# Kernel tuning notes

Measured on AMD Instinct MI355X. Metric: run time of the kernel, lower is better.

Reference implementation:

```python
import jax, jax.numpy as jnp
import numpy as np

N_S, N_G, E = 4000, 50000, 250000   # sample nodes, gene nodes, edges per relation
D, H, C1, C3 = 128, 4, 32, 64       # input dim, heads, layer-1 per-head dim, layer-3 per-head dim
NEG_SLOPE = 0.2


def gatv2(x_src, x_dst, src, dst, ea, Wl, bl, Wr, br, We, att, bias, n_dst, concat):
    """PyG GATv2Conv (add_self_loops=False, edge_dim=1, eval mode)."""
    Hh, C = att.shape
    xl = (x_src @ Wl + bl).reshape(-1, Hh, C)          # [N_src, H, C]
    xr = (x_dst @ Wr + br).reshape(-1, Hh, C)          # [N_dst, H, C]
    ee = (ea @ We).reshape(-1, Hh, C)                  # [E, H, C]
    m = jax.nn.leaky_relu(xl[src] + xr[dst] + ee, NEG_SLOPE)   # [E, H, C]
    logits = jnp.einsum('ehc,hc->eh', m, att)          # [E, H]
    # segment softmax over incoming edges of each destination node
    lmax = jax.ops.segment_max(logits, dst, num_segments=n_dst)[dst]
    ex = jnp.exp(logits - lmax)
    denom = jax.ops.segment_sum(ex, dst, num_segments=n_dst)[dst]
    alpha = ex / denom                                 # [E, H]
    out = jax.ops.segment_sum(xl[src] * alpha[:, :, None], dst, num_segments=n_dst)  # [N_dst, H, C]
    out = out.reshape(n_dst, Hh * C) if concat else out.mean(axis=1)
    return out + bias


def setup_inputs() -> dict:
    key = jax.random.key(0)
    ks = jax.random.split(key, 40)
    p = lambda i, shape: jax.random.normal(ks[i], shape, dtype=jnp.float32) * 0.05
    HC1, HC3 = H * C1, H * C3
    inp = {
        'x_mrna': p(0, (N_S, D)),
        'x_gene': p(1, (N_G, D)),
        'sg_src': jax.random.randint(ks[2], (E,), 0, N_S),
        'sg_dst': jax.random.randint(ks[3], (E,), 0, N_G),
        'gs_src': jax.random.randint(ks[4], (E,), 0, N_G),
        'gs_dst': jax.random.randint(ks[5], (E,), 0, N_S),
        'ea_sg': p(6, (E, 1)),
        'ea_gs': p(7, (E, 1)),
        # layer-1 GATv2 params, relation mrna->gene
        'Wl1_sg': p(8, (D, HC1)), 'bl1_sg': p(9, (HC1,)),
        'Wr1_sg': p(10, (D, HC1)), 'br1_sg': p(11, (HC1,)),
        'We1_sg': p(12, (1, HC1)), 'att1_sg': p(13, (H, C1)), 'bo1_sg': p(14, (HC1,)),
        # layer-1 GATv2 params, relation gene->mrna
        'Wl1_gs': p(15, (D, HC1)), 'bl1_gs': p(16, (HC1,)),
        'Wr1_gs': p(17, (D, HC1)), 'br1_gs': p(18, (HC1,)),
        'We1_gs': p(19, (1, HC1)), 'att1_gs': p(20, (H, C1)), 'bo1_gs': p(21, (HC1,)),
        # layer-3 GATv2 params, relation gene->mrna (concat=False)
        'Wl3_gs': p(22, (HC1, HC3)), 'bl3_gs': p(23, (HC3,)),
        'Wr3_gs': p(24, (HC1, HC3)), 'br3_gs': p(25, (HC3,)),
        'We3_gs': p(26, (1, HC3)), 'att3_gs': p(27, (H, C3)), 'bo3_gs': p(28, (C3,)),
        # self-loop linears for omic ('mrna') nodes
        'Wsl1': p(29, (D, C1)), 'bsl1': p(30, (C1,)),
        'Wsl3': p(31, (HC1, C3)), 'bsl3': p(32, (C3,)),
    }
    return inp


def reference(x_mrna, x_gene, sg_src, sg_dst, gs_src, gs_dst, ea_sg, ea_gs,
              Wl1_sg, bl1_sg, Wr1_sg, br1_sg, We1_sg, att1_sg, bo1_sg,
              Wl1_gs, bl1_gs, Wr1_gs, br1_gs, We1_gs, att1_gs, bo1_gs,
              Wl3_gs, bl3_gs, Wr3_gs, br3_gs, We3_gs, att3_gs, bo3_gs,
              Wsl1, bsl1, Wsl3, bsl3):
    # ---- layer 1 (HeteroConv over both relations) ----
    x1_gene = gatv2(x_mrna, x_gene, sg_src, sg_dst, ea_sg,
                    Wl1_sg, bl1_sg, Wr1_sg, br1_sg, We1_sg, att1_sg, bo1_sg, N_G, True)
    x1_mrna = gatv2(x_gene, x_mrna, gs_src, gs_dst, ea_gs,
                    Wl1_gs, bl1_gs, Wr1_gs, br1_gs, We1_gs, att1_gs, bo1_gs, N_S, True)
    # self-loop linear on omic nodes, repeated across heads (repeat(1, heads))
    x1_mrna = x1_mrna + jnp.tile(x_mrna @ Wsl1 + bsl1, (1, H))
    x1_mrna = jax.nn.relu(x1_mrna)
    x1_gene = jax.nn.relu(x1_gene)
    # ---- three_layers=False: x2 = x1; layer 3 (concat=False, head mean) ----
    x3_mrna = gatv2(x1_gene, x1_mrna, gs_src, gs_dst, ea_gs,
                    Wl3_gs, bl3_gs, Wr3_gs, br3_gs, We3_gs, att3_gs, bo3_gs, N_S, False)
    x3_mrna = x3_mrna + (x1_mrna @ Wsl3 + bsl3)
    x3_mrna = jax.nn.relu(x3_mrna)
    # integrator=None, single omic view -> squeeze to [N_S, C3]
    return x3_mrna
```

## Files before the change

### kernel.cpp

```cpp
#include <hip/hip_runtime.h>
#include <cstdint>
#include <cstddef>

#define NS 4000
#define NG 50000
#define NE 250000
#define DIM 128
#define NDST_TOT (NG + NS)

typedef __bf16 bf16_t;
typedef bf16_t bf16x8 __attribute__((ext_vector_type(8)));
typedef bf16_t bf16x4 __attribute__((ext_vector_type(4)));
typedef bf16_t bf16x2 __attribute__((ext_vector_type(2)));
typedef float floatx4 __attribute__((ext_vector_type(4)));

#define HIST_B 977
#define WT_TOT 143360
#define XM_W 64000
#define XG_W 800000
#define PREP_B 3935
struct HPArgs {
  const int* sgd; const int* gsd;
  int* cnt; unsigned short* rank_sg; unsigned short* rank_gs;
  const float* W[8]; bf16_t* Wt[8]; int N[8]; int e0[8];
  const float* xm; bf16_t* xbm;
  const float* xg; bf16_t* xbg;
};

__global__ __launch_bounds__(256) void histprep(HPArgs a) {
  if (blockIdx.x < HIST_B) {
    int e = blockIdx.x * 256 + threadIdx.x;
    if (e < NE) {
      a.rank_sg[e] = (unsigned short)atomicAdd(a.cnt + a.sgd[e], 1);
      a.rank_gs[e] = (unsigned short)atomicAdd(a.cnt + NG + a.gsd[e], 1);
    }
  } else {
    int u = (blockIdx.x - HIST_B) * 256 + threadIdx.x;
    if (u < WT_TOT) {
      int c = 0;
#pragma unroll
      for (int i = 1; i < 8; i++) if (u >= a.e0[i]) c = i;
      int idx = u - a.e0[c];
      int N = a.N[c];
      int k = idx / N, n = idx - k * N;
      a.Wt[c][n * 128 + k] = (bf16_t)a.W[c][idx];
    } else if (u < WT_TOT + XM_W) {
      int j = (u - WT_TOT) * 8;
      float4 v0 = *reinterpret_cast<const float4*>(a.xm + j);
      float4 v1 = *reinterpret_cast<const float4*>(a.xm + j + 4);
      bf16x8 b;
      b[0] = (bf16_t)v0.x; b[1] = (bf16_t)v0.y; b[2] = (bf16_t)v0.z; b[3] = (bf16_t)v0.w;
      b[4] = (bf16_t)v1.x; b[5] = (bf16_t)v1.y; b[6] = (bf16_t)v1.z; b[7] = (bf16_t)v1.w;
      *reinterpret_cast<bf16x8*>(a.xbm + j) = b;
    } else {
      int j = (u - WT_TOT - XM_W) * 8;
      float4 v0 = *reinterpret_cast<const float4*>(a.xg + j);
      float4 v1 = *reinterpret_cast<const float4*>(a.xg + j + 4);
      bf16x8 b;
      b[0] = (bf16_t)v0.x; b[1] = (bf16_t)v0.y; b[2] = (bf16_t)v0.z; b[3] = (bf16_t)v0.w;
      b[4] = (bf16_t)v1.x; b[5] = (bf16_t)v1.y; b[6] = (bf16_t)v1.z; b[7] = (bf16_t)v1.w;
      *reinterpret_cast<bf16x8*>(a.xbg + j) = b;
    }
  }
}

__global__ __launch_bounds__(1024) void scan1(const int* __restrict__ cnt,
                                              int* __restrict__ rp,
                                              int* __restrict__ csum, int n) {
  __shared__ int wsum[16];
  int i = blockIdx.x * 1024 + threadIdx.x;
  int lane = threadIdx.x & 63, w = threadIdx.x >> 6;
  int v = (i < n) ? cnt[i] : 0;
  int x = v;
#pragma unroll
  for (int off = 1; off < 64; off <<= 1) {
    int y = __shfl_up(x, off);
    if (lane >= off) x += y;
  }
  if (lane == 63) wsum[w] = x;
  __syncthreads();
  if (w == 0 && lane < 16) {
    int s = wsum[lane];
#pragma unroll
    for (int off = 1; off < 16; off <<= 1) {
      int y = __shfl_up(s, off);
      if (lane >= off) s += y;
    }
    wsum[lane] = s;
  }
  __syncthreads();
  int incl = x + (w ? wsum[w - 1] : 0);
  if (i < n) rp[i] = incl - v;
  if (threadIdx.x == 1023) csum[blockIdx.x] = incl;
}

__global__ __launch_bounds__(1024) void scan3(int* __restrict__ rp,
                                              const int* __restrict__ csum, int n) {
  __shared__ int pfx_s;
  if (threadIdx.x < 64) {
    int lane = threadIdx.x;
    int v = (lane < (int)blockIdx.x) ? csum[lane] : 0;
#pragma unroll
    for (int off = 32; off > 0; off >>= 1) v += __shfl_down(v, off);
    if (lane == 0) pfx_s = v;
  }
  __syncthreads();
  int i = blockIdx.x * 1024 + threadIdx.x;
  if (i < n) rp[i] += pfx_s;
  if (i == 0) rp[n] = 2 * NE;
}

#define SCAT_HALF 245
#define SCAT_B 490
struct SGArgs {
  const int* sgd; const int* gsd; const int* sgs; const int* gss;
  const float* easg; const float* eags;
  const int* rp; const unsigned short* rank_sg; const unsigned short* rank_gs;
  uint2* meta;
  const bf16_t* X[5];
  const bf16_t* Wt[5];
  const float* Bv[5];
  bf16_t* Y[5];
  int M[5];
  int Ncol[5];
  int blk0[5];
};

__global__ __launch_bounds__(256) void scatgemm(SGArgs a) {
  if (blockIdx.x < SCAT_B) {
    int rel = (int)blockIdx.x >= SCAT_HALF;
    int b = (int)blockIdx.x - (rel ? SCAT_HALF : 0);
    int t4 = (b * 256 + (int)threadIdx.x) * 4;
    if (t4 < NE) {
      const int* dp = rel ? a.gsd : a.sgd;
      const int* sp = rel ? a.gss : a.sgs;
      const float* ep = rel ? a.eags : a.easg;
      const unsigned short* rk = rel ? a.rank_gs : a.rank_sg;
      const int* rpb = a.rp + (rel ? NG : 0);
      int4 d4 = *reinterpret_cast<const int4*>(dp + t4);
      int4 s4 = *reinterpret_cast<const int4*>(sp + t4);
      float4 e4 = *reinterpret_cast<const float4*>(ep + t4);
      ushort4 r4 = *reinterpret_cast<const ushort4*>(rk + t4);
      int p0 = rpb[d4.x] + (int)r4.x;
      int p1 = rpb[d4.y] + (int)r4.y;
      int p2 = rpb[d4.z] + (int)r4.z;
      int p3 = rpb[d4.w] + (int)r4.w;
      uint2 v0, v1, v2, v3;
      v0.x = (unsigned)s4.x; v0.y = __float_as_uint(e4.x);
      v1.x = (unsigned)s4.y; v1.y = __float_as_uint(e4.y);
      v2.x = (unsigned)s4.z; v2.y = __float_as_uint(e4.z);
      v3.x = (unsigned)s4.w; v3.y = __float_as_uint(e4.w);
      a.meta[p0] = v0;
      a.meta[p1] = v1;
      a.meta[p2] = v2;
      a.meta[p3] = v3;
    }
    return;
  }
  int bid = blockIdx.x - SCAT_B;
  int c = 0;
#pragma unroll
  for (int i = 1; i < 5; i++) if (bid >= a.blk0[i]) c = i;
  const bf16_t* X = a.X[c];
  const bf16_t* Wt = a.Wt[c];
  const float* B = a.Bv[c];
  bf16_t* Y = a.Y[c];
  int M = a.M[c];
  int N = a.Ncol[c];

  int wv = threadIdx.x >> 6, lane = threadIdx.x & 63;
  int m16 = lane & 15, quad = lane >> 4;
  int row0 = (bid - a.blk0[c]) * 64 + wv * 16;
  int arow = row0 + m16;
  const bf16_t* xp = X + (size_t)arow * DIM + quad * 8;

  bf16x8 afrag[4];
#pragma unroll
  for (int kk = 0; kk < 4; kk++) {
    bf16x8 av = {};
    if (arow < M) av = *reinterpret_cast<const bf16x8*>(xp + kk * 32);
    afrag[kk] = av;
  }

  int ncols = N >> 4;
  for (int nt = 0; nt < ncols; nt++) {
    int col = nt * 16 + m16;
    const bf16_t* bptr = Wt + (size_t)col * DIM + quad * 8;
    floatx4 acc = {0.f, 0.f, 0.f, 0.f};
#pragma unroll
    for (int kk = 0; kk < 4; kk++) {
      bf16x8 b = *reinterpret_cast<const bf16x8*>(bptr + kk * 32);
      acc = __builtin_amdgcn_mfma_f32_16x16x32_bf16(afrag[kk], b, acc, 0, 0, 0);
    }
    float bias = B[col];
    int orow = row0 + quad * 4;
#pragma unroll
    for (int r = 0; r < 4; r++)
      if (orow + r < M) Y[(size_t)(orow + r) * N + col] = (bf16_t)(acc[r] + bias);
  }
}

template <int NCFG>
struct GArgs {
  const bf16_t* X[NCFG];
  const bf16_t* Wt[NCFG];
  const float* Bv[NCFG];
  bf16_t* Y[NCFG];
  int M[NCFG];
  int Ncol[NCFG];
  int blk0[NCFG];
};

template <int NCFG>
__global__ __launch_bounds__(256) void gemm_multi(GArgs<NCFG> a) {
  int c = 0;
#pragma unroll
  for (int i = 1; i < NCFG; i++) if ((int)blockIdx.x >= a.blk0[i]) c = i;
  const bf16_t* X = a.X[c];
  const bf16_t* Wt = a.Wt[c];
  const float* B = a.Bv[c];
  bf16_t* Y = a.Y[c];
  int M = a.M[c];
  int N = a.Ncol[c];

  int wv = threadIdx.x >> 6, lane = threadIdx.x & 63;
  int m16 = lane & 15, quad = lane >> 4;
  int row0 = (blockIdx.x - a.blk0[c]) * 64 + wv * 16;
  int arow = row0 + m16;
  const bf16_t* xp = X + (size_t)arow * DIM + quad * 8;

  bf16x8 afrag[4];
#pragma unroll
  for (int kk = 0; kk < 4; kk++) {
    bf16x8 av = {};
    if (arow < M) av = *reinterpret_cast<const bf16x8*>(xp + kk * 32);
    afrag[kk] = av;
  }

  int ncols = N >> 4;
  for (int nt = 0; nt < ncols; nt++) {
    int col = nt * 16 + m16;
    const bf16_t* bptr = Wt + (size_t)col * DIM + quad * 8;
    floatx4 acc = {0.f, 0.f, 0.f, 0.f};
#pragma unroll
    for (int kk = 0; kk < 4; kk++) {
      bf16x8 b = *reinterpret_cast<const bf16x8*>(bptr + kk * 32);
      acc = __builtin_amdgcn_mfma_f32_16x16x32_bf16(afrag[kk], b, acc, 0, 0, 0);
    }
    float bias = B[col];
    int orow = row0 + quad * 4;
#pragma unroll
    for (int r = 0; r < 4; r++)
      if (orow + r < M) Y[(size_t)(orow + r) * N + col] = (bf16_t)(acc[r] + bias);
  }
}

#define SGB 3125
__global__ __launch_bounds__(256) void gatC(
    const int* __restrict__ rp, const uint2* __restrict__ meta,
    const float* __restrict__ WeS, const float* __restrict__ attS,
    const float* __restrict__ boS,
    const bf16_t* __restrict__ xlS, const bf16_t* __restrict__ xrS,
    bf16_t* __restrict__ outS,
    const float* __restrict__ WeG, const float* __restrict__ attG,
    const float* __restrict__ boG,
    const bf16_t* __restrict__ xlG, const bf16_t* __restrict__ xrG,
    const bf16_t* __restrict__ slG, bf16_t* __restrict__ outG) {
  __shared__ uint2 smeta[256];
  __shared__ float lacc[16][128];
  __shared__ float lden[16][4];
  int lane = threadIdx.x & 63, wv = threadIdx.x >> 6;
  int gl = lane & 15, grp = lane >> 4;

  if (blockIdx.x < SGB) {
    int wid = blockIdx.x * 4 + wv;
    int d0 = wid * 4;
    int q = lane < 5 ? lane : 0;
    int rv = rp[d0 + q];
    int beg = __shfl(rv, grp), end = __shfl(rv, grp + 1);
    int dst = d0 + grp;

    float wev[8], atv[8], xrv[8], acc[8];
    *reinterpret_cast<float4*>(wev) = *reinterpret_cast<const float4*>(WeS + gl * 8);
    *reinterpret_cast<float4*>(wev + 4) = *reinterpret_cast<const float4*>(WeS + gl * 8 + 4);
    *reinterpret_cast<float4*>(atv) = *reinterpret_cast<const float4*>(attS + gl * 8);
    *reinterpret_cast<float4*>(atv + 4) = *reinterpret_cast<const float4*>(attS + gl * 8 + 4);
    bf16x8 xrb = *reinterpret_cast<const bf16x8*>(xrS + (size_t)dst * 128 + gl * 8);
#pragma unroll
    for (int v = 0; v < 8; v++) { xrv[v] = (float)xrb[v]; acc[v] = 0.f; }
    float den = 0.f;

    for (int i0 = beg; i0 < end; i0 += 16) {
      int cnt = min(16, end - i0);
      int s_l = 0; float ea_l = 0.f;
      if (gl < cnt) {
        uint2 mv = meta[i0 + gl];
        s_l = (int)mv.x; ea_l = __uint_as_float(mv.y);
      }
      int base = lane & 48;
      float ea = __shfl(ea_l, base);
      bf16x8 xlb = *reinterpret_cast<const bf16x8*>(
          xlS + (size_t)__shfl(s_l, base) * 128 + gl * 8);
      for (int k = 0; k < cnt; k++) {
        bf16x8 cur = xlb;
        float eac = ea;
        if (k + 1 < cnt) {
          ea = __shfl(ea_l, base + k + 1);
          xlb = *reinterpret_cast<const bf16x8*>(
              xlS + (size_t)__shfl(s_l, base + k + 1) * 128 + gl * 8);
        }
        float p = 0.f, xf[8];
#pragma unroll
        for (int v = 0; v < 8; v++) {
          xf[v] = (float)cur[v];
          float z = fmaf(eac, wev[v], xrv[v]) + xf[v];
          z = z > 0.f ? z : 0.2f * z;
          p = fmaf(z, atv[v], p);
        }
        p += __shfl_xor(p, 1);
        p += __shfl_xor(p, 2);
        float ex = __expf(p);
        den += ex;
#pragma unroll
        for (int v = 0; v < 8; v++) acc[v] = fmaf(ex, xf[v], acc[v]);
      }
    }
    float inv = den > 0.f ? 1.f / den : 0.f;
    bf16x8 o;
#pragma unroll
    for (int v = 0; v < 8; v++) {
      float val = acc[v] * inv + boS[gl * 8 + v];
      o[v] = (bf16_t)(val > 0.f ? val : 0.f);
    }
    *reinterpret_cast<bf16x8*>(outS + (size_t)dst * 128 + gl * 8) = o;
  } else {
    int d = (int)blockIdx.x - SGB;
    const int* rpg = rp + NG;
    int G = wv * 4 + grp;
    int tid = threadIdx.x;

    float wev[8], atv[8], xrv[8], acc[8];
    *reinterpret_cast<float4*>(wev) = *reinterpret_cast<const float4*>(WeG + gl * 8);
    *reinterpret_cast<float4*>(wev + 4) = *reinterpret_cast<const float4*>(WeG + gl * 8 + 4);
    *reinterpret_cast<float4*>(atv) = *reinterpret_cast<const float4*>(attG + gl * 8);
    *reinterpret_cast<float4*>(atv + 4) = *reinterpret_cast<const float4*>(attG + gl * 8 + 4);
    bf16x8 xrb = *reinterpret_cast<const bf16x8*>(xrG + (size_t)d * 128 + gl * 8);
#pragma unroll
    for (int v = 0; v < 8; v++) { xrv[v] = (float)xrb[v]; acc[v] = 0.f; }
    float den = 0.f;

    int beg = rpg[d], end = rpg[d + 1];
    for (int base = beg; base < end; base += 256) {
      int cntb = min(256, end - base);
      __syncthreads();
      if (tid < cntb) smeta[tid] = meta[base + tid];
      __syncthreads();
      int e = G;
      uint2 mv; bf16x8 xlb;
      if (e < cntb) {
        mv = smeta[e];
        xlb = *reinterpret_cast<const bf16x8*>(xlG + (size_t)mv.x * 128 + gl * 8);
      }
      while (e < cntb) {
        bf16x8 cur = xlb;
        float eac = __uint_as_float(mv.y);
        int en = e + 16;
        if (en < cntb) {
          mv = smeta[en];
          xlb = *reinterpret_cast<const bf16x8*>(xlG + (size_t)mv.x * 128 + gl * 8);
        }
        float p = 0.f, xf[8];
#pragma unroll
        for (int v = 0; v < 8; v++) {
          xf[v] = (float)cur[v];
          float z = fmaf(eac, wev[v], xrv[v]) + xf[v];
          z = z > 0.f ? z : 0.2f * z;
          p = fmaf(z, atv[v], p);
        }
        p += __shfl_xor(p, 1);
        p += __shfl_xor(p, 2);
        float ex = __expf(p);
        den += ex;
#pragma unroll
        for (int v = 0; v < 8; v++) acc[v] = fmaf(ex, xf[v], acc[v]);
        e = en;
      }
    }
#pragma unroll
    for (int v = 0; v < 8; v++) lacc[G][gl * 8 + v] = acc[v];
    if ((gl & 3) == 0) lden[G][gl >> 2] = den;
    __syncthreads();
    if (wv != 0) return;
    int ch = lane * 2;
    int h = lane >> 4;
    float a0 = 0.f, a1 = 0.f, dh = 0.f;
#pragma unroll
    for (int g2 = 0; g2 < 16; g2++) {
      a0 += lacc[g2][ch];
      a1 += lacc[g2][ch + 1];
      dh += lden[g2][h];
    }
    float inv = dh > 0.f ? 1.f / dh : 0.f;
    float v0 = a0 * inv + boG[ch] + (float)slG[(size_t)d * 32 + (ch & 31)];
    float v1 = a1 * inv + boG[ch + 1] + (float)slG[(size_t)d * 32 + ((ch + 1) & 31)];
    bf16x2 o;
    o[0] = (bf16_t)(v0 > 0.f ? v0 : 0.f);
    o[1] = (bf16_t)(v1 > 0.f ? v1 : 0.f);
    *reinterpret_cast<bf16x2*>(outG + (size_t)d * 128 + ch) = o;
  }
}

__global__ __launch_bounds__(256) void gatE(
    const int* __restrict__ rp, const uint2* __restrict__ meta,
    const float* __restrict__ We, const float* __restrict__ att,
    const bf16_t* __restrict__ xl, const bf16_t* __restrict__ xr,
    const float* __restrict__ bo, const bf16_t* __restrict__ sl,
    float* __restrict__ out) {
  __shared__ uint2 smeta[256];
  __shared__ float lacc[16][256];
  __shared__ float lden[16][4];
  int lane = threadIdx.x & 63, wv = threadIdx.x >> 6;
  int gl = lane & 15, grp = lane >> 4;
  int G = wv * 4 + grp;
  int tid = threadIdx.x;
  int d = blockIdx.x;

  float wev[16], atv[16], xrv[16], acc[16];
#pragma unroll
  for (int b = 0; b < 4; b++) {
    *reinterpret_cast<float4*>(wev + b * 4) =
        *reinterpret_cast<const float4*>(We + gl * 16 + b * 4);
    *reinterpret_cast<float4*>(atv + b * 4) =
        *reinterpret_cast<const float4*>(att + gl * 16 + b * 4);
  }
  {
    bf16x8 r0 = *reinterpret_cast<const bf16x8*>(xr + (size_t)d * 256 + gl * 16);
    bf16x8 r1 = *reinterpret_cast<const bf16x8*>(xr + (size_t)d * 256 + gl * 16 + 8);
#pragma unroll
    for (int v = 0; v < 8; v++) { xrv[v] = (float)r0[v]; xrv[v + 8] = (float)r1[v]; }
  }
#pragma unroll
  for (int v = 0; v < 16; v++) acc[v] = 0.f;
  float den = 0.f;

  int beg = rp[d], end = rp[d + 1];
  for (int base = beg; base < end; base += 256) {
    int cntb = min(256, end - base);
    __syncthreads();
    if (tid < cntb) smeta[tid] = meta[base + tid];
    __syncthreads();
    int e = G;
    uint2 mv; bf16x8 x0, x1;
    if (e < cntb) {
      mv = smeta[e];
      x0 = *reinterpret_cast<const bf16x8*>(xl + (size_t)mv.x * 256 + gl * 16);
      x1 = *reinterpret_cast<const bf16x8*>(xl + (size_t)mv.x * 256 + gl * 16 + 8);
    }
    while (e < cntb) {
      bf16x8 c0 = x0, c1 = x1;
      float eac = __uint_as_float(mv.y);
      int en = e + 16;
      if (en < cntb) {
        mv = smeta[en];
        x0 = *reinterpret_cast<const bf16x8*>(xl + (size_t)mv.x * 256 + gl * 16);
        x1 = *reinterpret_cast<const bf16x8*>(xl + (size_t)mv.x * 256 + gl * 16 + 8);
      }
      float p = 0.f, xf[16];
#pragma unroll
      for (int v = 0; v < 8; v++) { xf[v] = (float)c0[v]; xf[v + 8] = (float)c1[v]; }
#pragma unroll
      for (int v = 0; v < 16; v++) {
        float z = fmaf(eac, wev[v], xrv[v]) + xf[v];
        z = z > 0.f ? z : 0.2f * z;
        p = fmaf(z, atv[v], p);
      }
      p += __shfl_xor(p, 1);
      p += __shfl_xor(p, 2);
      float ex = __expf(p);
      den += ex;
#pragma unroll
      for (int v = 0; v < 16; v++) acc[v] = fmaf(ex, xf[v], acc[v]);
      e = en;
    }
  }
#pragma unroll
  for (int v = 0; v < 16; v++) lacc[G][gl * 16 + v] = acc[v];
  if ((gl & 3) == 0) lden[G][gl >> 2] = den;
  __syncthreads();
  if (wv != 0) return;
  int ch = lane * 4;
  int h = lane >> 4;
  float a[4] = {0.f, 0.f, 0.f, 0.f};
  float dh = 0.f;
#pragma unroll
  for (int g2 = 0; g2 < 16; g2++) {
#pragma unroll
    for (int v = 0; v < 4; v++) a[v] += lacc[g2][ch + v];
    dh += lden[g2][h];
  }
  float inv = dh > 0.f ? 1.f / dh : 0.f;
#pragma unroll
  for (int v = 0; v < 4; v++) {
    float s_ = a[v] * inv;
    s_ += __shfl_xor(s_, 16);
    s_ += __shfl_xor(s_, 32);
    if (lane < 16) {
      int c = (lane & 15) * 4 + v;
      float val = 0.25f * s_ + bo[c] + (float)sl[(size_t)d * 64 + c];
      out[(size_t)d * 64 + c] = val > 0.f ? val : 0.f;
    }
  }
}


static inline int nblk(long long threads) { return (int)((threads + 255) / 256); }
static inline int nrow(int M, int R) { return (M + R - 1) / R; }

extern "C" void kernel_launch(void* const* d_in, const int* in_sizes, int n_in,
                              void* d_out, int out_size, void* d_ws, size_t ws_size,
                              hipStream_t stream) {
  const float* x_mrna = (const float*)d_in[0];
  const float* x_gene = (const float*)d_in[1];
  const int* sg_src = (const int*)d_in[2];
  const int* sg_dst = (const int*)d_in[3];
  const int* gs_src = (const int*)d_in[4];
  const int* gs_dst = (const int*)d_in[5];
  const float* ea_sg = (const float*)d_in[6];
  const float* ea_gs = (const float*)d_in[7];
  const float* Wl1_sg = (const float*)d_in[8];
  const float* bl1_sg = (const float*)d_in[9];
  const float* Wr1_sg = (const float*)d_in[10];
  const float* br1_sg = (const float*)d_in[11];
  const float* We1_sg = (const float*)d_in[12];
  const float* att1_sg = (const float*)d_in[13];
  const float* bo1_sg = (const float*)d_in[14];
  const float* Wl1_gs = (const float*)d_in[15];
  const float* bl1_gs = (const float*)d_in[16];
  const float* Wr1_gs = (const float*)d_in[17];
  const float* br1_gs = (const float*)d_in[18];
  const float* We1_gs = (const float*)d_in[19];
  const float* att1_gs = (const float*)d_in[20];
  const float* bo1_gs = (const float*)d_in[21];
  const float* Wl3_gs = (const float*)d_in[22];
  const float* bl3_gs = (const float*)d_in[23];
  const float* Wr3_gs = (const float*)d_in[24];
  const float* br3_gs = (const float*)d_in[25];
  const float* We3_gs = (const float*)d_in[26];
  const float* att3_gs = (const float*)d_in[27];
  const float* bo3_gs = (const float*)d_in[28];
  const float* Wsl1 = (const float*)d_in[29];
  const float* bsl1 = (const float*)d_in[30];
  const float* Wsl3 = (const float*)d_in[31];
  const float* bsl3 = (const float*)d_in[32];

  float* ws = (float*)d_ws;
  bf16_t* xl1_gs = (bf16_t*)(ws + 0);
  bf16_t* xl1_sg = (bf16_t*)(ws + 3200000);
  bf16_t* xr1_sg = (bf16_t*)(ws + 3456000);
  bf16_t* xr1_gs = (bf16_t*)(ws + 6656000);
  bf16_t* xl3    = (bf16_t*)(ws + 0);
  bf16_t* xr3    = (bf16_t*)(ws + 6400000);
  bf16_t* xb_mrna = (bf16_t*)(ws + 6912000);
  bf16_t* xb_gene = (bf16_t*)(ws + 7168000);
  bf16_t* x1_gene = (bf16_t*)(ws + 10368000);
  bf16_t* x1_mrna = (bf16_t*)(ws + 13568000);
  bf16_t* sl1    = (bf16_t*)(ws + 13824000);
  bf16_t* sl3    = (bf16_t*)(ws + 13856000);
  int*   ib      = (int*)(ws + 13920000);
  int* cnt  = ib + 0;
  int* rpc  = ib + 54000;
  int* csum = ib + 108002;
  unsigned short* rank_sg = (unsigned short*)(ib + 108066);
  unsigned short* rank_gs = (unsigned short*)(ib + 233066);
  uint2* meta = (uint2*)(ib + 358066);
  bf16_t* wtb = (bf16_t*)(ib + 1358066);

  bf16_t* wt_l1sg = wtb + 0;
  bf16_t* wt_r1sg = wtb + 16384;
  bf16_t* wt_l1gs = wtb + 32768;
  bf16_t* wt_r1gs = wtb + 49152;
  bf16_t* wt_l3   = wtb + 65536;
  bf16_t* wt_r3   = wtb + 98304;
  bf16_t* wt_sl1  = wtb + 131072;
  bf16_t* wt_sl3  = wtb + 135168;

  hipMemsetAsync(cnt, 0, 54000 * sizeof(int), stream);

  {
    HPArgs hp;
    hp.sgd = sg_dst; hp.gsd = gs_dst;
    hp.cnt = cnt; hp.rank_sg = rank_sg; hp.rank_gs = rank_gs;
    const float* Wsrc[8] = {Wl1_sg, Wr1_sg, Wl1_gs, Wr1_gs, Wl3_gs, Wr3_gs, Wsl1, Wsl3};
    bf16_t* Wdst[8] = {wt_l1sg, wt_r1sg, wt_l1gs, wt_r1gs, wt_l3, wt_r3, wt_sl1, wt_sl3};
    int Nn[8] = {128, 128, 128, 128, 256, 256, 32, 64};
    int e0[8] = {0, 16384, 32768, 49152, 65536, 98304, 131072, 135168};
    for (int i = 0; i < 8; i++) { hp.W[i] = Wsrc[i]; hp.Wt[i] = Wdst[i]; hp.N[i] = Nn[i]; hp.e0[i] = e0[i]; }
    hp.xm = x_mrna; hp.xbm = xb_mrna;
    hp.xg = x_gene; hp.xbg = xb_gene;
    histprep<<<HIST_B + PREP_B, 256, 0, stream>>>(hp);
  }

  int nchunks = (NDST_TOT + 1023) / 1024;
  scan1<<<nchunks, 1024, 0, stream>>>(cnt, rpc, csum, NDST_TOT);
  scan3<<<nchunks, 1024, 0, stream>>>(rpc, csum, NDST_TOT);

  {
    SGArgs sa;
    sa.sgd = sg_dst; sa.gsd = gs_dst; sa.sgs = sg_src; sa.gss = gs_src;
    sa.easg = ea_sg; sa.eags = ea_gs;
    sa.rp = rpc; sa.rank_sg = rank_sg; sa.rank_gs = rank_gs; sa.meta = meta;
    const bf16_t* Xs[5] = {xb_mrna, xb_gene, xb_gene, xb_mrna, xb_mrna};
    const bf16_t* Ws[5] = {wt_l1sg, wt_r1sg, wt_l1gs, wt_r1gs, wt_sl1};
    const float* Bs[5] = {bl1_sg, br1_sg, bl1_gs, br1_gs, bsl1};
    bf16_t* Ys[5] = {xl1_sg, xr1_sg, xl1_gs, xr1_gs, sl1};
    int Ms[5] = {NS, NG, NG, NS, NS};
    int Ns[5] = {128, 128, 128, 128, 32};
    int b0 = 0;
    for (int i = 0; i < 5; i++) {
      sa.X[i] = Xs[i]; sa.Wt[i] = Ws[i]; sa.Bv[i] = Bs[i]; sa.Y[i] = Ys[i];
      sa.M[i] = Ms[i]; sa.Ncol[i] = Ns[i]; sa.blk0[i] = b0;
      b0 += nrow(Ms[i], 64);
    }
    scatgemm<<<SCAT_B + b0, 256, 0, stream>>>(sa);
  }

  gatC<<<SGB + NS, 256, 0, stream>>>(
      rpc, meta,
      We1_sg, att1_sg, bo1_sg, xl1_sg, xr1_sg, x1_gene,
      We1_gs, att1_gs, bo1_gs, xl1_gs, xr1_gs, sl1, x1_mrna);

  {
    GArgs<3> ga;
    const bf16_t* Xs[3] = {x1_gene, x1_mrna, x1_mrna};
    const bf16_t* Ws[3] = {wt_l3, wt_r3, wt_sl3};
    const float* Bs[3] = {bl3_gs, br3_gs, bsl3};
    bf16_t* Ys[3] = {xl3, xr3, sl3};
    int Ms[3] = {NG, NS, NS};
    int Ns[3] = {256, 256, 64};
    int b0 = 0;
    for (int i = 0; i < 3; i++) {
      ga.X[i] = Xs[i]; ga.Wt[i] = Ws[i]; ga.Bv[i] = Bs[i]; ga.Y[i] = Ys[i];
      ga.M[i] = Ms[i]; ga.Ncol[i] = Ns[i]; ga.blk0[i] = b0;
      b0 += nrow(Ms[i], 64);
    }
    gemm_multi<3><<<b0, 256, 0, stream>>>(ga);
  }

  gatE<<<NS, 256, 0, stream>>>(rpc + NG, meta, We3_gs, att3_gs,
                               xl3, xr3, bo3_gs, sl3, (float*)d_out);
}
```

Baseline: 298.2 us.

## Register-block GEMM rows per wave and swap MFMA operands for vector stores

Each wave in the two fused GEMM kernels now covers 4 (scatgemm) or 2 (gemm_multi) 16-row tiles, so every weight fragment loaded is reused across several row tiles. The MFMA operands are swapped so each lane holds 4 consecutive output columns. That lets the bias come in as one float4 load and the output be written as one packed bf16x4 store instead of four strided scalar stores. Launch grids shrink to match, and launch bounds request 4 blocks per CU. The cost is more registers and fewer blocks, which may hurt load balance on the smaller matrices.

```diff
diff --git a/kernel.cpp b/kernel.cpp
--- a/kernel.cpp
+++ b/kernel.cpp
@@ -126,7 +126,7 @@
   int blk0[5];
 };
 
-__global__ __launch_bounds__(256) void scatgemm(SGArgs a) {
+__global__ __launch_bounds__(256, 4) void scatgemm(SGArgs a) {
   if (blockIdx.x < SCAT_B) {
     int rel = (int)blockIdx.x >= SCAT_HALF;
     int b = (int)blockIdx.x - (rel ? SCAT_HALF : 0);
@@ -170,33 +170,45 @@
 
   int wv = threadIdx.x >> 6, lane = threadIdx.x & 63;
   int m16 = lane & 15, quad = lane >> 4;
-  int row0 = (bid - a.blk0[c]) * 64 + wv * 16;
-  int arow = row0 + m16;
-  const bf16_t* xp = X + (size_t)arow * DIM + quad * 8;
-
-  bf16x8 afrag[4];
-#pragma unroll
-  for (int kk = 0; kk < 4; kk++) {
-    bf16x8 av = {};
-    if (arow < M) av = *reinterpret_cast<const bf16x8*>(xp + kk * 32);
-    afrag[kk] = av;
+  int wrow0 = (bid - a.blk0[c]) * 256 + wv * 64;
+
+  bf16x8 afrag[4][4];
+#pragma unroll
+  for (int rt = 0; rt < 4; rt++) {
+    int arow = wrow0 + rt * 16 + m16;
+    const bf16_t* xp = X + (size_t)arow * DIM + quad * 8;
+#pragma unroll
+    for (int kk = 0; kk < 4; kk++) {
+      bf16x8 av = {};
+      if (arow < M) av = *reinterpret_cast<const bf16x8*>(xp + kk * 32);
+      afrag[rt][kk] = av;
+    }
   }
 
   int ncols = N >> 4;
   for (int nt = 0; nt < ncols; nt++) {
-    int col = nt * 16 + m16;
-    const bf16_t* bptr = Wt + (size_t)col * DIM + quad * 8;
-    floatx4 acc = {0.f, 0.f, 0.f, 0.f};
-#pragma unroll
-    for (int kk = 0; kk < 4; kk++) {
-      bf16x8 b = *reinterpret_cast<const bf16x8*>(bptr + kk * 32);
-      acc = __builtin_amdgcn_mfma_f32_16x16x32_bf16(afrag[kk], b, acc, 0, 0, 0);
-    }
-    float bias = B[col];
-    int orow = row0 + quad * 4;
-#pragma unroll
-    for (int r = 0; r < 4; r++)
-      if (orow + r < M) Y[(size_t)(orow + r) * N + col] = (bf16_t)(acc[r] + bias);
+    const bf16_t* bptr = Wt + (size_t)(nt * 16 + m16) * DIM + quad * 8;
+    bf16x8 bfrag[4];
+#pragma unroll
+    for (int kk = 0; kk < 4; kk++)
+      bfrag[kk] = *reinterpret_cast<const bf16x8*>(bptr + kk * 32);
+    float4 bias = *reinterpret_cast<const float4*>(B + nt * 16 + quad * 4);
+#pragma unroll
+    for (int rt = 0; rt < 4; rt++) {
+      floatx4 acc = {0.f, 0.f, 0.f, 0.f};
+#pragma unroll
+      for (int kk = 0; kk < 4; kk++)
+        acc = __builtin_amdgcn_mfma_f32_16x16x32_bf16(bfrag[kk], afrag[rt][kk], acc, 0, 0, 0);
+      int row = wrow0 + rt * 16 + m16;
+      if (row < M) {
+        bf16x4 o;
+        o[0] = (bf16_t)(acc[0] + bias.x);
+        o[1] = (bf16_t)(acc[1] + bias.y);
+        o[2] = (bf16_t)(acc[2] + bias.z);
+        o[3] = (bf16_t)(acc[3] + bias.w);
+        *reinterpret_cast<bf16x4*>(Y + (size_t)row * N + nt * 16 + quad * 4) = o;
+      }
+    }
   }
 }
 
@@ -212,7 +224,7 @@
 };
 
 template <int NCFG>
-__global__ __launch_bounds__(256) void gemm_multi(GArgs<NCFG> a) {
+__global__ __launch_bounds__(256, 4) void gemm_multi(GArgs<NCFG> a) {
   int c = 0;
 #pragma unroll
   for (int i = 1; i < NCFG; i++) if ((int)blockIdx.x >= a.blk0[i]) c = i;
@@ -225,33 +237,45 @@
 
   int wv = threadIdx.x >> 6, lane = threadIdx.x & 63;
   int m16 = lane & 15, quad = lane >> 4;
-  int row0 = (blockIdx.x - a.blk0[c]) * 64 + wv * 16;
-  int arow = row0 + m16;
-  const bf16_t* xp = X + (size_t)arow * DIM + quad * 8;
-
-  bf16x8 afrag[4];
-#pragma unroll
-  for (int kk = 0; kk < 4; kk++) {
-    bf16x8 av = {};
-    if (arow < M) av = *reinterpret_cast<const bf16x8*>(xp + kk * 32);
-    afrag[kk] = av;
+  int wrow0 = ((int)blockIdx.x - a.blk0[c]) * 128 + wv * 32;
+
+  bf16x8 afrag[2][4];
+#pragma unroll
+  for (int rt = 0; rt < 2; rt++) {
+    int arow = wrow0 + rt * 16 + m16;
+    const bf16_t* xp = X + (size_t)arow * DIM + quad * 8;
+#pragma unroll
+    for (int kk = 0; kk < 4; kk++) {
+      bf16x8 av = {};
+      if (arow < M) av = *reinterpret_cast<const bf16x8*>(xp + kk * 32);
+      afrag[rt][kk] = av;
+    }
   }
 
   int ncols = N >> 4;
   for (int nt = 0; nt < ncols; nt++) {
-    int col = nt * 16 + m16;
-    const bf16_t* bptr = Wt + (size_t)col * DIM + quad * 8;
-    floatx4 acc = {0.f, 0.f, 0.f, 0.f};
-#pragma unroll
-    for (int kk = 0; kk < 4; kk++) {
-      bf16x8 b = *reinterpret_cast<const bf16x8*>(bptr + kk * 32);
-      acc = __builtin_amdgcn_mfma_f32_16x16x32_bf16(afrag[kk], b, acc, 0, 0, 0);
-    }
-    float bias = B[col];
-    int orow = row0 + quad * 4;
-#pragma unroll
-    for (int r = 0; r < 4; r++)
-      if (orow + r < M) Y[(size_t)(orow + r) * N + col] = (bf16_t)(acc[r] + bias);
+    const bf16_t* bptr = Wt + (size_t)(nt * 16 + m16) * DIM + quad * 8;
+    bf16x8 bfrag[4];
+#pragma unroll
+    for (int kk = 0; kk < 4; kk++)
+      bfrag[kk] = *reinterpret_cast<const bf16x8*>(bptr + kk * 32);
+    float4 bias = *reinterpret_cast<const float4*>(B + nt * 16 + quad * 4);
+#pragma unroll
+    for (int rt = 0; rt < 2; rt++) {
+      floatx4 acc = {0.f, 0.f, 0.f, 0.f};
+#pragma unroll
+      for (int kk = 0; kk < 4; kk++)
+        acc = __builtin_amdgcn_mfma_f32_16x16x32_bf16(bfrag[kk], afrag[rt][kk], acc, 0, 0, 0);
+      int row = wrow0 + rt * 16 + m16;
+      if (row < M) {
+        bf16x4 o;
+        o[0] = (bf16_t)(acc[0] + bias.x);
+        o[1] = (bf16_t)(acc[1] + bias.y);
+        o[2] = (bf16_t)(acc[2] + bias.z);
+        o[3] = (bf16_t)(acc[3] + bias.w);
+        *reinterpret_cast<bf16x4*>(Y + (size_t)row * N + nt * 16 + quad * 4) = o;
+      }
+    }
   }
 }
 
@@ -619,7 +643,7 @@
     for (int i = 0; i < 5; i++) {
       sa.X[i] = Xs[i]; sa.Wt[i] = Ws[i]; sa.Bv[i] = Bs[i]; sa.Y[i] = Ys[i];
       sa.M[i] = Ms[i]; sa.Ncol[i] = Ns[i]; sa.blk0[i] = b0;
-      b0 += nrow(Ms[i], 64);
+      b0 += nrow(Ms[i], 256);
     }
     scatgemm<<<SCAT_B + b0, 256, 0, stream>>>(sa);
   }
@@ -641,7 +665,7 @@
     for (int i = 0; i < 3; i++) {
       ga.X[i] = Xs[i]; ga.Wt[i] = Ws[i]; ga.Bv[i] = Bs[i]; ga.Y[i] = Ys[i];
       ga.M[i] = Ms[i]; ga.Ncol[i] = Ns[i]; ga.blk0[i] = b0;
-      b0 += nrow(Ms[i], 64);
+      b0 += nrow(Ms[i], 128);
     }
     gemm_multi<3><<<b0, 256, 0, stream>>>(ga);
   }
```

Measured after the change: 278.1 us. 6.7% less time.
